# Performance work log

Measured on AMD Instinct MI355X. Metric: run time of the kernel, lower is better.

The kernel has to match this reference:

```python
import jax, jax.numpy as jnp
import numpy as np

IN_C = 128
HIDE_C = 256
HC2 = HIDE_C // 2
OUT_C = 128
WS = 7          # winsize
SCALE = 0.125   # 1/8
EPS = 1e-5      # BatchNorm eps
B, H, W = 32, 112, 112


def setup_inputs() -> dict:
    key = jax.random.key(0)
    ks = jax.random.split(key, 24)
    f32 = jnp.float32

    def w(k, shape):
        return jax.random.normal(k, shape, f32) * 0.05

    def bn_params(k, c):
        k1, k2, k3, k4 = jax.random.split(k, 4)
        gamma = 1.0 + 0.1 * jax.random.normal(k1, (c,), f32)
        beta = 0.1 * jax.random.normal(k2, (c,), f32)
        mean = 0.1 * jax.random.normal(k3, (c,), f32)
        var = jax.random.uniform(k4, (c,), f32, 0.5, 1.5)
        return gamma, beta, mean, var

    x = jax.random.normal(ks[0], (B, IN_C, H, W), f32)
    wq = w(ks[1], (HC2, IN_C))
    gq, bq, mq, vq = bn_params(ks[2], HC2)
    wk = w(ks[3], (HC2, IN_C))
    gk, bk, mk, vk = bn_params(ks[4], HC2)
    wv = w(ks[5], (HIDE_C, IN_C))
    gv, bv, mv, vv = bn_params(ks[6], HIDE_C)
    wo = w(ks[7], (OUT_C, HIDE_C))
    bo = 0.05 * jax.random.normal(ks[8], (OUT_C,), f32)
    go, bbo, mo, vo = bn_params(ks[9], OUT_C)
    return {"x": x,
            "wq": wq, "gq": gq, "bq": bq, "mq": mq, "vq": vq,
            "wk": wk, "gk": gk, "bk": bk, "mk": mk, "vk": vk,
            "wv": wv, "gv": gv, "bv": bv, "mv": mv, "vv": vv,
            "wo": wo, "bo": bo, "go": go, "bbo": bbo, "mo": mo, "vo": vo}


def _conv1x1(x, w):
    # 1x1 conv, stride 1, no bias: pure channel contraction
    return jnp.einsum('bchw,oc->bohw', x, w)


def _bn(x, g, b, m, v):
    # inference-mode BatchNorm2d
    p = lambda a: a[None, :, None, None]
    return p(g) * (x - p(m)) * jax.lax.rsqrt(p(v) + EPS) + p(b)


def _to_windows(t):
    # 'b c (h1 ws1) (w1 ws2) -> b (c ws1 ws2) (h1 w1)'
    b, c, h, w = t.shape
    h1, w1 = h // WS, w // WS
    t = t.reshape(b, c, h1, WS, w1, WS).transpose(0, 1, 3, 5, 2, 4)
    return t.reshape(b, c * WS * WS, h1 * w1)


def _forward(x, wq, gq, bq, mq, vq, wk, gk, bk, mk, vk,
             wv, gv, bv, mv, vv, wo, bo, go, bbo, mo, vo):
    q = _bn(_conv1x1(x, wq), gq, bq, mq, vq)   # [B, HC2, H, W]
    k = _bn(_conv1x1(x, wk), gk, bk, mk, vk)   # [B, HC2, H, W]
    v = _bn(_conv1x1(x, wv), gv, bv, mv, vv)   # [B, HIDE_C, H, W]
    b, _, h, w = q.shape
    h1, w1 = h // WS, w // WS

    qf = _to_windows(q)  # [B, HC2*49, h1*w1]
    kf = _to_windows(k)
    vf = _to_windows(v)  # [B, HIDE_C*49, h1*w1]

    dots = jnp.einsum('bci,bcj->bij', qf, kf) * SCALE   # [B, T, T], T=h1*w1
    attn = jax.nn.softmax(dots, axis=-1)
    out = jnp.einsum('bij,bdj->bid', attn, vf)          # [B, T, HIDE_C*49]

    # 'b (h1 w1) (c1 ws1 ws2) -> b c1 (h1 ws1) (w1 ws2)'
    out = out.reshape(b, h1, w1, HIDE_C, WS, WS).transpose(0, 3, 1, 4, 2, 5)
    out = out.reshape(b, HIDE_C, h, w)

    out = jax.nn.gelu(out, approximate=False)
    out = _conv1x1(out, wo) + bo[None, :, None, None]
    out = _bn(out, go, bbo, mo, vo)
    # dropout is identity in eval; downsample is identity (stride=1, in_c==out_c)
    return jax.nn.gelu(out + x, approximate=False)


def reference(x, wq, gq, bq, mq, vq, wk, gk, bk, mk, vk,
              wv, gv, bv, mv, vv, wo, bo, go, bbo, mo, vo):
    return _forward(x, wq, gq, bq, mq, vq, wk, gk, bk, mk, vk,
                    wv, gv, bv, mv, vv, wo, bo, go, bbo, mo, vo)
```

## Files before the change

### kernel.cpp

```cpp
#include <hip/hip_runtime.h>


typedef unsigned short u16;
typedef unsigned int u32;
typedef short s16x8 __attribute__((ext_vector_type(8)));
typedef float f32x4 __attribute__((ext_vector_type(4)));
typedef u16 u16x8 __attribute__((ext_vector_type(8)));
typedef u16 u16x4 __attribute__((ext_vector_type(4)));

#define EPSV 1e-5f

__device__ __forceinline__ float bf2f(u16 h) {
  u32 u = ((u32)h) << 16;
  return __builtin_bit_cast(float, u);
}
__device__ __forceinline__ u16 f2bf(float f) {
  u32 u = __builtin_bit_cast(u32, f);
  u += 0x7FFFu + ((u >> 16) & 1u);
  return (u16)(u >> 16);
}
__device__ __forceinline__ s16x8 ld8(const u16* p) { return *(const s16x8*)p; }
__device__ __forceinline__ f32x4 mfma_bf16(s16x8 a, s16x8 b, f32x4 c) {
  return __builtin_amdgcn_mfma_f32_16x16x32_bf16(a, b, c, 0, 0, 0);
}
__device__ __forceinline__ float gelu_f(float v) {
  float e = exp2f(-2.3022083f * (v + 0.044715f * v * v * v));
  return v / (1.0f + e);
}

__global__ void k_params(
    const float* __restrict__ gq, const float* __restrict__ bq, const float* __restrict__ mq, const float* __restrict__ vq,
    const float* __restrict__ gk, const float* __restrict__ bk, const float* __restrict__ mk, const float* __restrict__ vk,
    const float* __restrict__ gv, const float* __restrict__ bv, const float* __restrict__ mv, const float* __restrict__ vv,
    const float* __restrict__ bo, const float* __restrict__ go, const float* __restrict__ bbo, const float* __restrict__ mo,
    const float* __restrict__ vo,
    float* __restrict__ sc512, float* __restrict__ sh512, float* __restrict__ sco, float* __restrict__ sho)
{
  const int i = threadIdx.x;
  if (i < 128) {
    const float s = gq[i] * rsqrtf(vq[i] + EPSV);
    sc512[i] = s;
    sh512[i] = bq[i] - mq[i] * s;
    const float so = go[i] * rsqrtf(vo[i] + EPSV);
    sco[i] = so;
    sho[i] = (bo[i] - mo[i]) * so + bbo[i];
  } else if (i < 256) {
    const int c = i - 128;
    const float s = gk[c] * rsqrtf(vk[c] + EPSV);
    sc512[i] = s;
    sh512[i] = bk[c] - mk[c] * s;
  } else if (i < 512) {
    const int c = i - 256;
    const float s = gv[c] * rsqrtf(vv[c] + EPSV);
    sc512[i] = s;
    sh512[i] = bv[c] - mv[c] * s;
  }
}

__global__ void k_wconv(const float* __restrict__ wq, const float* __restrict__ wk,
                        const float* __restrict__ wv, const float* __restrict__ sc512,
                        u16* __restrict__ wfused)
{
  const int idx4 = (blockIdx.x * 256 + threadIdx.x) * 4;
  const int co = idx4 >> 7, c = idx4 & 127;
  const float* src = (co < 128) ? (wq + co * 128 + c)
                   : (co < 256) ? (wk + (co - 128) * 128 + c)
                                : (wv + (co - 256) * 128 + c);
  const float s = sc512[co];
  const float4 v = *(const float4*)src;
  u16x4 r;
  r[0] = f2bf(v.x * s); r[1] = f2bf(v.y * s);
  r[2] = f2bf(v.z * s); r[3] = f2bf(v.w * s);
  *(u16x4*)(wfused + idx4) = r;
}

__global__ __launch_bounds__(256, 2) void k_qkv(
    const float* __restrict__ x, const u16* __restrict__ wfused,
    const float* __restrict__ sh512,
    u16* __restrict__ QW, u16* __restrict__ KW, u16* __restrict__ VW)
{
  __shared__ u16 XT[256 * 128];
  const int b = blockIdx.y;
  const int px0 = blockIdx.x * 256;
  const int t = threadIdx.x;

  {
    const float* xp = x + (size_t)b * 128u * 12544u + (size_t)(px0 + t);
    const int sw = (t & 15) << 3;
    #pragma unroll 8
    for (int c = 0; c < 128; c += 4) {
      u16x4 pk;
      pk[0] = f2bf(xp[(size_t)(c + 0) * 12544u]);
      pk[1] = f2bf(xp[(size_t)(c + 1) * 12544u]);
      pk[2] = f2bf(xp[(size_t)(c + 2) * 12544u]);
      pk[3] = f2bf(xp[(size_t)(c + 3) * 12544u]);
      *(u16x4*)&XT[t * 128 + (c ^ sw)] = pk;
    }
  }
  __syncthreads();

  const int w = t >> 6, l = t & 63, a15 = l & 15, g = l >> 4;

  s16x8 af[4][4];
  #pragma unroll
  for (int pxt = 0; pxt < 4; ++pxt) {
    const int row = w * 64 + pxt * 16 + a15;
    const int sw = (row & 15) << 3;
    #pragma unroll
    for (int ks = 0; ks < 4; ++ks) {
      const int cc = ks * 32 + g * 8;
      af[pxt][ks] = *(const s16x8*)&XT[row * 128 + (cc ^ sw)];
    }
  }

  u32 qkidx[4][4], vidx[4][4];
  #pragma unroll
  for (int pxt = 0; pxt < 4; ++pxt) {
    #pragma unroll
    for (int r = 0; r < 4; ++r) {
      const int px = px0 + w * 64 + pxt * 16 + g * 4 + r;
      const int hh = px / 112, ww = px - hh * 112;
      const int h1 = hh / 7, p = hh - h1 * 7;
      const int w1 = ww / 7, q = ww - w1 * 7;
      const int j = h1 * 16 + w1, pq = p * 7 + q;
      qkidx[pxt][r] = ((u32)(b * 256 + j) * 49u + (u32)pq) * 128u;
      vidx[pxt][r] = (u32)(b * 256 + j) * 12544u + (u32)(pq * 256);
    }
  }

  #pragma unroll 1
  for (int cot = 0; cot < 32; ++cot) {
    const int co = cot * 16 + a15;
    const u16* wrow = wfused + (u32)co * 128u;
    s16x8 bfr[4];
    #pragma unroll
    for (int ks = 0; ks < 4; ++ks) bfr[ks] = ld8(wrow + ks * 32 + g * 8);

    f32x4 acc[4];
    #pragma unroll
    for (int pxt = 0; pxt < 4; ++pxt) { acc[pxt][0]=0.f; acc[pxt][1]=0.f; acc[pxt][2]=0.f; acc[pxt][3]=0.f; }
    #pragma unroll
    for (int ks = 0; ks < 4; ++ks)
      #pragma unroll
      for (int pxt = 0; pxt < 4; ++pxt)
        acc[pxt] = mfma_bf16(af[pxt][ks], bfr[ks], acc[pxt]);

    const float sh = sh512[co];
    if (cot < 8) {
      #pragma unroll
      for (int pxt = 0; pxt < 4; ++pxt)
        #pragma unroll
        for (int r = 0; r < 4; ++r)
          QW[qkidx[pxt][r] + (u32)co] = f2bf(acc[pxt][r] + sh);
    } else if (cot < 16) {
      #pragma unroll
      for (int pxt = 0; pxt < 4; ++pxt)
        #pragma unroll
        for (int r = 0; r < 4; ++r)
          KW[qkidx[pxt][r] + (u32)(co - 128)] = f2bf(acc[pxt][r] + sh);
    } else {
      #pragma unroll
      for (int pxt = 0; pxt < 4; ++pxt)
        #pragma unroll
        for (int r = 0; r < 4; ++r)
          VW[vidx[pxt][r] + (u32)(co - 256)] = f2bf(acc[pxt][r] + sh);
    }
  }
}

__global__ __launch_bounds__(512, 2) void k_dots(
    const u16* __restrict__ QW, const u16* __restrict__ KW, float* __restrict__ Pp)
{
  __shared__ u16 QS[256 * 64];
  __shared__ u16 KS[256 * 64];
  const int b = blockIdx.y, ks = blockIdx.x;
  const int nch = (ks == 7) ? 14 : 12;
  const int t = threadIdx.x;
  const int w = t >> 6, l = t & 63, a15 = l & 15, g = l >> 4;
  const int i0w = (w >> 1) * 64, j0w = (w & 1) * 128;

  f32x4 acc[4][8];
  #pragma unroll
  for (int i = 0; i < 4; ++i)
    #pragma unroll
    for (int j = 0; j < 8; ++j) { acc[i][j][0]=0.f; acc[i][j][1]=0.f; acc[i][j][2]=0.f; acc[i][j][3]=0.f; }

  const int srow = t >> 1;
  const int sgr0 = (t & 1) * 4;
  const size_t kb = (size_t)ks * 768 + (size_t)((t & 1) * 32);
  const u16* qsrc = QW + ((size_t)b * 256 + srow) * 6272 + kb;
  const u16* ksrc = KW + ((size_t)b * 256 + srow) * 6272 + kb;
  u16* qdst = &QS[srow * 64];
  u16* kdst = &KS[srow * 64];
  const int swr = srow & 7;

  for (int ch = 0; ch < nch; ++ch) {
    const int k0 = ch * 64;
    #pragma unroll
    for (int gi = 0; gi < 4; ++gi) {
      const int off = ((sgr0 + gi) ^ swr) << 3;
      *(u16x8*)(qdst + off) = *(const u16x8*)(qsrc + k0 + gi * 8);
      *(u16x8*)(kdst + off) = *(const u16x8*)(ksrc + k0 + gi * 8);
    }
    __syncthreads();
    #pragma unroll
    for (int kk = 0; kk < 2; ++kk) {
      s16x8 af[4], bfr[8];
      #pragma unroll
      for (int i4 = 0; i4 < 4; ++i4) {
        const int ir = i0w + i4 * 16 + a15;
        af[i4] = *(const s16x8*)&QS[ir * 64 + (((kk * 4 + g) ^ (ir & 7)) << 3)];
      }
      #pragma unroll
      for (int j8 = 0; j8 < 8; ++j8) {
        const int jr = j0w + j8 * 16 + a15;
        bfr[j8] = *(const s16x8*)&KS[jr * 64 + (((kk * 4 + g) ^ (jr & 7)) << 3)];
      }
      #pragma unroll
      for (int i4 = 0; i4 < 4; ++i4)
        #pragma unroll
        for (int j8 = 0; j8 < 8; ++j8)
          acc[i4][j8] = mfma_bf16(af[i4], bfr[j8], acc[i4][j8]);
    }
    __syncthreads();
  }

  float* pp = Pp + ((size_t)ks * 32 + b) * 256 * 256;
  #pragma unroll
  for (int i4 = 0; i4 < 4; ++i4)
    #pragma unroll
    for (int r = 0; r < 4; ++r) {
      const int ir = i0w + i4 * 16 + g * 4 + r;
      #pragma unroll
      for (int j8 = 0; j8 < 8; ++j8)
        pp[(size_t)ir * 256 + j0w + j8 * 16 + a15] = acc[i4][j8][r];
    }
}

__global__ __launch_bounds__(256, 4) void k_smax(const float* __restrict__ Pp, u16* __restrict__ P)
{
  const int b = blockIdx.y, it = blockIdx.x;
  const int t = threadIdx.x;
  const int row = it * 32 + (t >> 3);
  const int cg = t & 7;
  const size_t rb = ((size_t)b * 256 + row) * 256 + cg * 32;

  f32x4 s[8];
  #pragma unroll
  for (int cc = 0; cc < 8; ++cc) { s[cc][0]=0.f; s[cc][1]=0.f; s[cc][2]=0.f; s[cc][3]=0.f; }
  #pragma unroll 1
  for (int ks = 0; ks < 8; ++ks) {
    const float* src = Pp + (size_t)ks * 32 * 256 * 256 + rb;
    #pragma unroll
    for (int cc = 0; cc < 8; ++cc)
      s[cc] += *(const f32x4*)(src + cc * 4);
  }
  float m = -1e30f;
  #pragma unroll
  for (int cc = 0; cc < 8; ++cc)
    m = fmaxf(m, fmaxf(fmaxf(s[cc][0], s[cc][1]), fmaxf(s[cc][2], s[cc][3])));
  m = fmaxf(m, __shfl_xor(m, 1));
  m = fmaxf(m, __shfl_xor(m, 2));
  m = fmaxf(m, __shfl_xor(m, 4));
  const float CEXP = 0.18033688f;
  float sum = 0.f;
  #pragma unroll
  for (int cc = 0; cc < 8; ++cc)
    #pragma unroll
    for (int e = 0; e < 4; ++e) {
      const float p = exp2f((s[cc][e] - m) * CEXP);
      s[cc][e] = p;
      sum += p;
    }
  sum += __shfl_xor(sum, 1);
  sum += __shfl_xor(sum, 2);
  sum += __shfl_xor(sum, 4);
  const float inv = 1.0f / sum;
  u16* dst = P + rb;
  #pragma unroll
  for (int cc = 0; cc < 8; cc += 2) {
    u16x8 o;
    o[0] = f2bf(s[cc][0] * inv);     o[1] = f2bf(s[cc][1] * inv);
    o[2] = f2bf(s[cc][2] * inv);     o[3] = f2bf(s[cc][3] * inv);
    o[4] = f2bf(s[cc + 1][0] * inv); o[5] = f2bf(s[cc + 1][1] * inv);
    o[6] = f2bf(s[cc + 1][2] * inv); o[7] = f2bf(s[cc + 1][3] * inv);
    *(u16x8*)(dst + cc * 4) = o;
  }
}

__global__ __launch_bounds__(512, 2) void k_pv(
    const u16* __restrict__ P, const u16* __restrict__ VW, u16* __restrict__ GN)
{
  __shared__ u16 VT[256 * 64];
  __shared__ u16 PS[256 * 64];
  const int b = blockIdx.y, pq = blockIdx.x;
  const int t = threadIdx.x;
  const int w = t >> 6, l = t & 63, a15 = l & 15, g = l >> 4;
  const int m0w = (w >> 1) * 64, i0w = (w & 1) * 128;

  f32x4 acc[4][8];
  #pragma unroll
  for (int i = 0; i < 4; ++i)
    #pragma unroll
    for (int j = 0; j < 8; ++j) { acc[i][j][0]=0.f; acc[i][j][1]=0.f; acc[i][j][2]=0.f; acc[i][j][3]=0.f; }

  const int sj0 = (t & 7) * 8;
  const int sm0 = (t >> 3) * 4;
  const u16* vbase = VW + ((size_t)b * 256 + sj0) * 12544 + pq * 256 + sm0;
  const int prow = t >> 1;
  const int pgr0 = (t & 1) * 4;
  const u16* pbase = P + ((size_t)b * 256 + prow) * 256 + (t & 1) * 32;
  u16* psdst = &PS[prow * 64];
  const int pswr = prow & 7;

  for (int jc = 0; jc < 4; ++jc) {
    const int j0 = jc * 64;
    u16x4 rr[8];
    #pragma unroll
    for (int ji = 0; ji < 8; ++ji)
      rr[ji] = *(const u16x4*)(vbase + (size_t)(j0 + ji) * 12544);
    #pragma unroll
    for (int mi = 0; mi < 4; ++mi) {
      u16x8 wv;
      #pragma unroll
      for (int ji = 0; ji < 8; ++ji) wv[ji] = rr[ji][mi];
      const int m = sm0 + mi;
      *(u16x8*)&VT[m * 64 + (((sj0 >> 3) ^ (m & 7)) << 3)] = wv;
    }
    #pragma unroll
    for (int gi = 0; gi < 4; ++gi) {
      const int off = ((pgr0 + gi) ^ pswr) << 3;
      *(u16x8*)(psdst + off) = *(const u16x8*)(pbase + j0 + gi * 8);
    }
    __syncthreads();
    #pragma unroll
    for (int kk = 0; kk < 2; ++kk) {
      s16x8 av[4], bp[8];
      #pragma unroll
      for (int mf = 0; mf < 4; ++mf) {
        const int m = m0w + mf * 16 + a15;
        av[mf] = *(const s16x8*)&VT[m * 64 + (((kk * 4 + g) ^ (m & 7)) << 3)];
      }
      #pragma unroll
      for (int f = 0; f < 8; ++f) {
        const int i = i0w + f * 16 + a15;
        bp[f] = *(const s16x8*)&PS[i * 64 + (((kk * 4 + g) ^ (i & 7)) << 3)];
      }
      #pragma unroll
      for (int mf = 0; mf < 4; ++mf)
        #pragma unroll
        for (int f = 0; f < 8; ++f)
          acc[mf][f] = mfma_bf16(av[mf], bp[f], acc[mf][f]);
    }
    __syncthreads();
  }

  const int pp_ = pq / 7, qq = pq - 7 * pp_;
  #pragma unroll
  for (int f = 0; f < 8; ++f) {
    const int i = i0w + f * 16 + a15;
    const int h1 = i >> 4, w1 = i & 15;
    const size_t gb = ((size_t)b * 12544 + (size_t)((h1 * 7 + pp_) * 112 + w1 * 7 + qq)) * 256;
    #pragma unroll
    for (int mf = 0; mf < 4; ++mf) {
      u16x4 st;
      #pragma unroll
      for (int r = 0; r < 4; ++r) st[r] = f2bf(gelu_f(acc[mf][f][r]));
      *(u16x4*)&GN[gb + m0w + mf * 16 + g * 4] = st;
    }
  }
}

__global__ __launch_bounds__(512, 2) void k_out(
    const u16* __restrict__ GN, const float* __restrict__ wo,
    const float* __restrict__ x, const float* __restrict__ sco,
    const float* __restrict__ sho, float* __restrict__ out)
{
  __shared__ u16 WO[128 * 256];
  __shared__ u16 OT[128 * 264];
  const int b = blockIdx.y;
  const int px0 = blockIdx.x * 256;
  const int t = threadIdx.x;
  const int w = t >> 6, l = t & 63, a15 = l & 15, g = l >> 4;

  {
    const int o = t >> 2, gr0 = (t & 3) * 8;
    const float s = sco[o];
    const float* src = wo + o * 256 + gr0 * 8;
    u16* dr = &WO[o * 256];
    #pragma unroll
    for (int gi = 0; gi < 8; ++gi) {
      const float4 v0 = *(const float4*)(src + gi * 8);
      const float4 v1 = *(const float4*)(src + gi * 8 + 4);
      u16x8 pk;
      pk[0] = f2bf(v0.x * s); pk[1] = f2bf(v0.y * s);
      pk[2] = f2bf(v0.z * s); pk[3] = f2bf(v0.w * s);
      pk[4] = f2bf(v1.x * s); pk[5] = f2bf(v1.y * s);
      pk[6] = f2bf(v1.z * s); pk[7] = f2bf(v1.w * s);
      *(u16x8*)(dr + (((gr0 + gi) ^ (o & 7)) << 3)) = pk;
    }
  }
  __syncthreads();

  const int pw = w >> 1, ow = w & 1;
  const int o0w = ow * 64;
  f32x4 acc[4][4];
  #pragma unroll
  for (int i = 0; i < 4; ++i)
    #pragma unroll
    for (int j = 0; j < 4; ++j) { acc[i][j][0]=0.f; acc[i][j][1]=0.f; acc[i][j][2]=0.f; acc[i][j][3]=0.f; }

  #pragma unroll 1
  for (int ksl = 0; ksl < 8; ++ksl) {
    s16x8 af[4], bw[4];
    #pragma unroll
    for (int pxf = 0; pxf < 4; ++pxf) {
      const int row = px0 + pw * 64 + pxf * 16 + a15;
      af[pxf] = ld8(GN + ((size_t)b * 12544 + row) * 256 + ksl * 32 + g * 8);
    }
    #pragma unroll
    for (int of = 0; of < 4; ++of) {
      const int o = o0w + of * 16 + a15;
      bw[of] = *(const s16x8*)&WO[o * 256 + (((ksl * 4 + g) ^ (o & 7)) << 3)];
    }
    #pragma unroll
    for (int pxf = 0; pxf < 4; ++pxf)
      #pragma unroll
      for (int of = 0; of < 4; ++of)
        acc[pxf][of] = mfma_bf16(af[pxf], bw[of], acc[pxf][of]);
  }

  #pragma unroll
  for (int pxf = 0; pxf < 4; ++pxf)
    #pragma unroll
    for (int of = 0; of < 4; ++of) {
      u16x4 st;
      #pragma unroll
      for (int r = 0; r < 4; ++r) st[r] = f2bf(acc[pxf][of][r]);
      *(u16x4*)&OT[(o0w + of * 16 + a15) * 264 + pw * 64 + pxf * 16 + g * 4] = st;
    }
  __syncthreads();

  const int o2 = t >> 2;
  const float sh = sho[o2];
  const size_t xb = ((size_t)b * 128 + o2) * 12544 + px0;
  #pragma unroll 2
  for (int ii = 0; ii < 16; ++ii) {
    const int po = ii * 16 + (t & 3) * 4;
    const u16x4 zt = *(const u16x4*)&OT[o2 * 264 + po];
    const float4 xv = *(const float4*)(x + xb + po);
    float4 r;
    r.x = gelu_f(bf2f(zt[0]) + sh + xv.x);
    r.y = gelu_f(bf2f(zt[1]) + sh + xv.y);
    r.z = gelu_f(bf2f(zt[2]) + sh + xv.z);
    r.w = gelu_f(bf2f(zt[3]) + sh + xv.w);
    *(float4*)(out + xb + po) = r;
  }
}

extern "C" void kernel_launch(void* const* d_in, const int* in_sizes, int n_in,
                              void* d_out, int out_size, void* d_ws, size_t ws_size,
                              hipStream_t stream) {
  (void)in_sizes; (void)n_in; (void)out_size; (void)ws_size;
  const float* x   = (const float*)d_in[0];
  const float* wq  = (const float*)d_in[1];
  const float* gq  = (const float*)d_in[2];
  const float* bq  = (const float*)d_in[3];
  const float* mq  = (const float*)d_in[4];
  const float* vq  = (const float*)d_in[5];
  const float* wk  = (const float*)d_in[6];
  const float* gk  = (const float*)d_in[7];
  const float* bk  = (const float*)d_in[8];
  const float* mk  = (const float*)d_in[9];
  const float* vk  = (const float*)d_in[10];
  const float* wv  = (const float*)d_in[11];
  const float* gv  = (const float*)d_in[12];
  const float* bv  = (const float*)d_in[13];
  const float* mv  = (const float*)d_in[14];
  const float* vv  = (const float*)d_in[15];
  const float* wo  = (const float*)d_in[16];
  const float* bo  = (const float*)d_in[17];
  const float* go  = (const float*)d_in[18];
  const float* bbo = (const float*)d_in[19];
  const float* mo  = (const float*)d_in[20];
  const float* vo  = (const float*)d_in[21];

  u16* QW = (u16*)d_ws;
  u16* KW = QW + 51380224u;
  u16* VW = KW + 51380224u;
  u16* GN = VW + 102760448u;
  u16* P  = QW;
  float* Pp = (float*)GN;
  u16* wfused = GN;
  float* sc512 = (float*)(GN + 102760448u);
  float* sh512 = sc512 + 512;
  float* sco = sh512 + 512;
  float* sho = sco + 128;

  k_params<<<1, 512, 0, stream>>>(gq, bq, mq, vq, gk, bk, mk, vk, gv, bv, mv, vv,
                                  bo, go, bbo, mo, vo, sc512, sh512, sco, sho);
  k_wconv<<<64, 256, 0, stream>>>(wq, wk, wv, sc512, wfused);
  k_qkv<<<dim3(49, 32), 256, 0, stream>>>(x, wfused, sh512, QW, KW, VW);
  k_dots<<<dim3(8, 32), 512, 0, stream>>>(QW, KW, Pp);
  k_smax<<<dim3(8, 32), 256, 0, stream>>>(Pp, P);
  k_pv<<<dim3(49, 32), 512, 0, stream>>>(P, VW, GN);
  k_out<<<dim3(49, 32), 512, 0, stream>>>(GN, wo, x, sco, sho, (float*)d_out);
}
```

Measured before the change: 748.8 us.

## Stage QKV projection outputs in LDS for coalesced row-contiguous global writes

```diff
diff --git a/kernel.cpp b/kernel.cpp
--- a/kernel.cpp
+++ b/kernel.cpp
@@ -112,59 +112,64 @@
       af[pxt][ks] = *(const s16x8*)&XT[row * 128 + (cc ^ sw)];
     }
   }
-
-  u32 qkidx[4][4], vidx[4][4];
-  #pragma unroll
-  for (int pxt = 0; pxt < 4; ++pxt) {
-    #pragma unroll
-    for (int r = 0; r < 4; ++r) {
-      const int px = px0 + w * 64 + pxt * 16 + g * 4 + r;
-      const int hh = px / 112, ww = px - hh * 112;
-      const int h1 = hh / 7, p = hh - h1 * 7;
-      const int w1 = ww / 7, q = ww - w1 * 7;
-      const int j = h1 * 16 + w1, pq = p * 7 + q;
-      qkidx[pxt][r] = ((u32)(b * 256 + j) * 49u + (u32)pq) * 128u;
-      vidx[pxt][r] = (u32)(b * 256 + j) * 12544u + (u32)(pq * 256);
-    }
-  }
+  __syncthreads();
+
+  const int px = px0 + t;
+  const int hh = px / 112, ww = px - hh * 112;
+  const int h1 = hh / 7, p = hh - h1 * 7;
+  const int w1 = ww / 7, q = ww - w1 * 7;
+  const int j = h1 * 16 + w1, pq = p * 7 + q;
+  u16* const qrow = QW + ((size_t)(b * 256 + j) * 49 + pq) * 128;
+  u16* const krow = KW + ((size_t)(b * 256 + j) * 49 + pq) * 128;
+  u16* const vrow = VW + (size_t)(b * 256 + j) * 12544 + pq * 256;
 
   #pragma unroll 1
-  for (int cot = 0; cot < 32; ++cot) {
-    const int co = cot * 16 + a15;
-    const u16* wrow = wfused + (u32)co * 128u;
-    s16x8 bfr[4];
-    #pragma unroll
-    for (int ks = 0; ks < 4; ++ks) bfr[ks] = ld8(wrow + ks * 32 + g * 8);
-
-    f32x4 acc[4];
-    #pragma unroll
-    for (int pxt = 0; pxt < 4; ++pxt) { acc[pxt][0]=0.f; acc[pxt][1]=0.f; acc[pxt][2]=0.f; acc[pxt][3]=0.f; }
-    #pragma unroll
-    for (int ks = 0; ks < 4; ++ks)
-      #pragma unroll
-      for (int pxt = 0; pxt < 4; ++pxt)
-        acc[pxt] = mfma_bf16(af[pxt][ks], bfr[ks], acc[pxt]);
-
-    const float sh = sh512[co];
-    if (cot < 8) {
-      #pragma unroll
-      for (int pxt = 0; pxt < 4; ++pxt)
+  for (int phase = 0; phase < 4; ++phase) {
+    s16x8 bcur[4];
+    {
+      const u16* wrow = wfused + (u32)(phase * 128 + a15) * 128u;
+      #pragma unroll
+      for (int ks = 0; ks < 4; ++ks) bcur[ks] = ld8(wrow + ks * 32 + g * 8);
+    }
+    #pragma unroll 1
+    for (int cot8 = 0; cot8 < 8; ++cot8) {
+      s16x8 bnext[4];
+      if (cot8 < 7) {
+        const u16* wrow = wfused + (u32)(phase * 128 + (cot8 + 1) * 16 + a15) * 128u;
         #pragma unroll
-        for (int r = 0; r < 4; ++r)
-          QW[qkidx[pxt][r] + (u32)co] = f2bf(acc[pxt][r] + sh);
-    } else if (cot < 16) {
-      #pragma unroll
-      for (int pxt = 0; pxt < 4; ++pxt)
+        for (int ks = 0; ks < 4; ++ks) bnext[ks] = ld8(wrow + ks * 32 + g * 8);
+      }
+      f32x4 acc[4];
+      #pragma unroll
+      for (int pxt = 0; pxt < 4; ++pxt) { acc[pxt][0]=0.f; acc[pxt][1]=0.f; acc[pxt][2]=0.f; acc[pxt][3]=0.f; }
+      #pragma unroll
+      for (int ks = 0; ks < 4; ++ks)
         #pragma unroll
-        for (int r = 0; r < 4; ++r)
-          KW[qkidx[pxt][r] + (u32)(co - 128)] = f2bf(acc[pxt][r] + sh);
-    } else {
-      #pragma unroll
-      for (int pxt = 0; pxt < 4; ++pxt)
+        for (int pxt = 0; pxt < 4; ++pxt)
+          acc[pxt] = mfma_bf16(af[pxt][ks], bcur[ks], acc[pxt]);
+
+      const float sh = sh512[phase * 128 + cot8 * 16 + a15];
+      const int co = cot8 * 16 + a15;
+      #pragma unroll
+      for (int pxt = 0; pxt < 4; ++pxt) {
         #pragma unroll
-        for (int r = 0; r < 4; ++r)
-          VW[vidx[pxt][r] + (u32)(co - 256)] = f2bf(acc[pxt][r] + sh);
-    }
+        for (int r = 0; r < 4; ++r) {
+          const int pxl = w * 64 + pxt * 16 + g * 4 + r;
+          XT[pxl * 128 + (co ^ ((pxl & 15) << 3))] = f2bf(acc[pxt][r] + sh);
+        }
+      }
+      #pragma unroll
+      for (int ks = 0; ks < 4; ++ks) bcur[ks] = bnext[ks];
+    }
+    __syncthreads();
+    {
+      u16* dst = (phase == 0) ? qrow : (phase == 1) ? krow : vrow + (phase - 2) * 128;
+      const int sw = (t & 15) << 3;
+      #pragma unroll
+      for (int c8 = 0; c8 < 16; ++c8)
+        *(u16x8*)(dst + c8 * 8) = *(const u16x8*)&XT[t * 128 + ((c8 * 8) ^ sw)];
+    }
+    __syncthreads();
   }
 }
 
```

After: 743.0 us. Within noise of the previous version (-0.8%).
